# Optimization experiments

Hardware: AMD Instinct MI355X
Metric: run time of the kernel (lower is better)

## Reference

```python
import jax, jax.numpy as jnp
import numpy as np
from jax import lax

C = 64  # filters, reduction=1


def setup_inputs() -> dict:
    key = jax.random.key(0)
    k = jax.random.split(key, 5)
    B, H, W = 16, 64, 64
    x = jax.random.normal(k[0], (B, C, H, W), dtype=jnp.float32)
    # conv_du params (PyTorch Conv2d default init scale ~ U(-s,s), s=1/sqrt(fan_in))
    s = 1.0 / np.sqrt(C * 9)
    w1 = jax.random.uniform(k[1], (C, C, 3, 3), jnp.float32, -s, s)
    b1 = jax.random.uniform(k[2], (C,), jnp.float32, -s, s)
    w2 = jax.random.uniform(k[3], (C, C, 3, 3), jnp.float32, -s, s)
    b2 = jax.random.uniform(k[4], (C,), jnp.float32, -s, s)
    return {"x": x, "w1": w1, "b1": b1, "w2": w2, "b2": b2}


def _normalize_cov(cov, iterN=5):
    # Newton-Schulz iteration for matrix square root, as in SOCA.normalizeCov
    B, ch = cov.shape[0], cov.shape[-1]
    I3 = 3.0 * jnp.eye(ch, dtype=cov.dtype)[None]  # [1,ch,ch], broadcasts over batch
    # normA = 1/3 * sum(cov @ 3I) = sum(cov) per batch
    normA = jnp.sum(cov, axis=(1, 2))  # [B]
    A = cov / normA[:, None, None]
    ZY = 0.5 * (I3 - A)
    Y = jnp.matmul(A, ZY)
    Z = ZY
    for _ in range(1, iterN - 1):  # iterations 1..iterN-2
        ZY = 0.5 * (I3 - jnp.matmul(Z, Y))
        Y = jnp.matmul(Y, ZY)
        Z = jnp.matmul(ZY, Z)
    ZY = 0.5 * jnp.matmul(Y, I3 - jnp.matmul(Z, Y))
    y = ZY * jnp.sqrt(normA)[:, None, None]
    y = jnp.mean(y, axis=1).reshape(B, ch, 1, 1)  # mean over rows -> channel descriptor
    return y


def _conv_same(x, w, b):
    out = lax.conv_general_dilated(
        x, w, window_strides=(1, 1), padding="SAME",
        dimension_numbers=("NCHW", "OIHW", "NCHW"))
    return out + b[None, :, None, None]


def reference(x, w1, b1, w2, b2):
    B, c, h, w = x.shape
    M = h * w
    xf = x.reshape(B, c, M)
    Minv = 1.0 / M
    # I_hat = (1/M) * (I - (1/M) * ones)  -- centering matrix, materialized as in source
    I_hat = Minv * (jnp.eye(M, dtype=x.dtype) - Minv * jnp.ones((M, M), dtype=x.dtype))
    cov = jnp.matmul(jnp.matmul(xf, I_hat), jnp.swapaxes(xf, 1, 2))  # [B,c,c]
    y_cov = _normalize_cov(cov, 5)  # [B,c,1,1]
    y = _conv_same(y_cov, w1, b1)
    y = jax.nn.relu(y)
    y = _conv_same(y, w2, b2)
    y = jax.nn.sigmoid(y)
    return y * x
```

## Files before the change

kernel.cpp:

```cpp
#include <hip/hip_runtime.h>
#include <math.h>

#define KS 16
#define CHUNK 256
#define PART_STRIDE 4160

typedef __attribute__((ext_vector_type(8))) short short8;
typedef __attribute__((ext_vector_type(4))) float floatx4;

__device__ __forceinline__ unsigned short f2bf(float f) {
    unsigned int u = __float_as_uint(f);
    return (unsigned short)((u + 0x7fffu + ((u >> 16) & 1u)) >> 16);
}
__device__ __forceinline__ float bf2f(unsigned short h) {
    return __uint_as_float(((unsigned int)h) << 16);
}
__device__ __forceinline__ int HW(int r, int kb) {
    return ((kb << 6) + (r ^ (kb & 15))) << 3;
}
__device__ __forceinline__ floatx4 mfma_bf16(short8 a, short8 b, floatx4 c) {
    return __builtin_amdgcn_mfma_f32_16x16x32_bf16(a, b, c, 0, 0, 0);
}

__global__ __launch_bounds__(256) void cov_partial_kernel(const float* __restrict__ x,
                                                          float* __restrict__ ws) {
    __shared__ __align__(16) unsigned short xh[64 * CHUNK];
    __shared__ __align__(16) unsigned short xl[64 * CHUNK];
    __shared__ float rs_part[4][64];
    int blk = blockIdx.x, b = blk >> 4, ks = blk & 15;
    int tid = threadIdx.x, lane = tid & 63, wv = tid >> 6;
    const float* xb = x + ((size_t)b * 64) * 4096 + ks * CHUNK;

    int kbw = lane >> 1, wsub = (lane & 1) << 2;
    #pragma unroll
    for (int r = 0; r < 16; ++r) {
        int c = wv * 16 + r;
        float4 v = *reinterpret_cast<const float4*>(xb + (size_t)c * 4096 + lane * 4);
        float vv[4] = {v.x, v.y, v.z, v.w};
        unsigned short hs[4], ls[4];
        #pragma unroll
        for (int q = 0; q < 4; ++q) {
            hs[q] = f2bf(vv[q]);
            ls[q] = f2bf(vv[q] - bf2f(hs[q]));
        }
        int idx = HW(c, kbw) + wsub;
        uint2 u;
        u.x = hs[0] | ((unsigned)hs[1] << 16); u.y = hs[2] | ((unsigned)hs[3] << 16);
        *reinterpret_cast<uint2*>(&xh[idx]) = u;
        u.x = ls[0] | ((unsigned)ls[1] << 16); u.y = ls[2] | ((unsigned)ls[3] << 16);
        *reinterpret_cast<uint2*>(&xl[idx]) = u;
    }
    __syncthreads();

    int g = lane >> 4, rh = lane & 15;
    int ta0 = (wv >> 1) << 1, tc0 = (wv & 1) << 1;
    floatx4 acc[2][2];
    #pragma unroll
    for (int a = 0; a < 2; ++a)
        #pragma unroll
        for (int c = 0; c < 2; ++c)
            acc[a][c] = (floatx4){0.f, 0.f, 0.f, 0.f};

    #pragma unroll
    for (int ks_ = 0; ks_ < 8; ++ks_) {
        int kb = ks_ * 4 + g;
        short8 ah[2], al[2], bh[2], bl[2];
        #pragma unroll
        for (int a = 0; a < 2; ++a) {
            int o = HW(16 * (ta0 + a) + rh, kb);
            ah[a] = *reinterpret_cast<const short8*>(&xh[o]);
            al[a] = *reinterpret_cast<const short8*>(&xl[o]);
        }
        #pragma unroll
        for (int c = 0; c < 2; ++c) {
            int o = HW(16 * (tc0 + c) + rh, kb);
            bh[c] = *reinterpret_cast<const short8*>(&xh[o]);
            bl[c] = *reinterpret_cast<const short8*>(&xl[o]);
        }
        #pragma unroll
        for (int a = 0; a < 2; ++a)
            #pragma unroll
            for (int c = 0; c < 2; ++c) {
                acc[a][c] = mfma_bf16(ah[a], bh[c], acc[a][c]);
                acc[a][c] = mfma_bf16(ah[a], bl[c], acc[a][c]);
                acc[a][c] = mfma_bf16(al[a], bh[c], acc[a][c]);
            }
    }

    float* outp = ws + (size_t)blk * PART_STRIDE;
    #pragma unroll
    for (int a = 0; a < 2; ++a)
        #pragma unroll
        for (int c = 0; c < 2; ++c) {
            int j = 16 * (tc0 + c) + rh;
            int i0 = 16 * (ta0 + a) + 4 * g;
            *reinterpret_cast<float4*>(&outp[j * 64 + i0]) =
                make_float4(acc[a][c][0], acc[a][c][1], acc[a][c][2], acc[a][c][3]);
        }

    {
        float s = 0.f;
        #pragma unroll
        for (int m = 0; m < 8; ++m) {
            int o = HW(lane, wv * 8 + m);
            short8 vh = *reinterpret_cast<const short8*>(&xh[o]);
            short8 vl = *reinterpret_cast<const short8*>(&xl[o]);
            #pragma unroll
            for (int e = 0; e < 8; ++e)
                s += bf2f((unsigned short)vh[e]) + bf2f((unsigned short)vl[e]);
        }
        rs_part[wv][lane] = s;
    }
    __syncthreads();
    if (tid < 64)
        outp[4096 + tid] = rs_part[0][tid] + rs_part[1][tid] + rs_part[2][tid] + rs_part[3][tid];
}

template <int MODE>
__device__ __forceinline__ void mm_pass(const unsigned short (*U)[4096],
                                        const unsigned short (*V)[4096],
                                        unsigned short (*D)[4096], int tid) {
    int lane = tid & 63, wv = tid >> 6;
    int g = lane >> 4, rh = lane & 15;
    int ta = wv & 3, tc0 = (wv >> 2) << 1;
    floatx4 acc[2];
    acc[0] = (floatx4){0.f, 0.f, 0.f, 0.f};
    acc[1] = (floatx4){0.f, 0.f, 0.f, 0.f};

    #pragma unroll
    for (int ks_ = 0; ks_ < 2; ++ks_) {
        int kb = ks_ * 4 + g;
        int ao = HW(16 * ta + rh, kb);
        short8 auh = *reinterpret_cast<const short8*>(&U[0][ao]);
        short8 aul = *reinterpret_cast<const short8*>(&U[1][ao]);
        #pragma unroll
        for (int c = 0; c < 2; ++c) {
            int bo = HW(16 * (tc0 + c) + rh, kb);
            short8 bvh = *reinterpret_cast<const short8*>(&V[0][bo]);
            short8 bvl = *reinterpret_cast<const short8*>(&V[1][bo]);
            acc[c] = mfma_bf16(auh, bvh, acc[c]);
            acc[c] = mfma_bf16(auh, bvl, acc[c]);
            acc[c] = mfma_bf16(aul, bvh, acc[c]);
        }
    }

    int kbi = 2 * ta + (g >> 1);
    int sub = (g & 1) << 2;
    #pragma unroll
    for (int c = 0; c < 2; ++c) {
        int j = 16 * (tc0 + c) + rh;
        unsigned short hs[4], ls[4];
        #pragma unroll
        for (int q = 0; q < 4; ++q) {
            int i = 16 * ta + 4 * g + q;
            float v = acc[c][q];
            if (MODE == 0) v = 0.5f * ((i == j ? 3.0f : 0.0f) - v);
            hs[q] = f2bf(v);
            ls[q] = f2bf(v - bf2f(hs[q]));
        }
        int idx = HW(j, kbi) + sub;
        uint2 u;
        u.x = hs[0] | ((unsigned)hs[1] << 16); u.y = hs[2] | ((unsigned)hs[3] << 16);
        *reinterpret_cast<uint2*>(&D[0][idx]) = u;
        u.x = ls[0] | ((unsigned)ls[1] << 16); u.y = ls[2] | ((unsigned)ls[3] << 16);
        *reinterpret_cast<uint2*>(&D[1][idx]) = u;
    }
    __syncthreads();
}

__global__ __launch_bounds__(512) void ns_kernel(const float* __restrict__ wsin,
                                                 const float* __restrict__ w1,
                                                 const float* __restrict__ b1,
                                                 const float* __restrict__ w2,
                                                 const float* __restrict__ b2,
                                                 float* __restrict__ s_out) {
    __shared__ __align__(16) float buf[4096];
    __shared__ __align__(16) unsigned short planes[5][2][4096];
    __shared__ float w1t[64 * 65];
    __shared__ float w2t[64 * 65];
    __shared__ float red[512];
    __shared__ float part[8][64];
    __shared__ float rsum[64], uvec[64], tvec[64], wvec[64], ych[64], hid[64];
    int b = blockIdx.x, tid = threadIdx.x;

    {
        int o = tid & 63, g8 = tid >> 6;
        #pragma unroll
        for (int q = 0; q < 8; ++q) {
            int i = g8 * 8 + q;
            w1t[i * 65 + o] = w1[(o * 64 + i) * 9 + 4];
            w2t[i * 65 + o] = w2[(o * 64 + i) * 9 + 4];
        }
    }

    const float* base = wsin + (size_t)b * KS * PART_STRIDE;
    #pragma unroll
    for (int r = 0; r < 2; ++r) {
        int e = (r * 512 + tid) * 4;
        floatx4 s4 = (floatx4){0.f, 0.f, 0.f, 0.f};
        for (int k = 0; k < KS; ++k)
            s4 += *reinterpret_cast<const floatx4*>(base + k * PART_STRIDE + e);
        *reinterpret_cast<floatx4*>(&buf[e]) = s4;
    }
    if (tid < 64) {
        float s = 0.f;
        for (int k = 0; k < KS; ++k) s += base[k * PART_STRIDE + 4096 + tid];
        rsum[tid] = s;
    }
    __syncthreads();

    const float invM = 1.0f / 4096.0f;
    float lsum = 0.f;
    #pragma unroll
    for (int r = 0; r < 2; ++r) {
        int e = (r * 512 + tid) * 4;
        int i = e >> 6, j = e & 63;
        floatx4 cv = *reinterpret_cast<const floatx4*>(&buf[e]);
        float mui = rsum[i] * invM;
        #pragma unroll
        for (int q = 0; q < 4; ++q) cv[q] = cv[q] * invM - mui * (rsum[j + q] * invM);
        *reinterpret_cast<floatx4*>(&buf[e]) = cv;
        lsum += cv[0] + cv[1] + cv[2] + cv[3];
    }
    red[tid] = lsum;
    __syncthreads();
    for (int s = 256; s > 0; s >>= 1) {
        if (tid < s) red[tid] += red[tid + s];
        __syncthreads();
    }
    const float normA = red[0];
    const float invNA = 1.0f / normA;

    {
        int r = tid >> 3, oct = tid & 7;
        short8 ah, al, zh, zl;
        #pragma unroll
        for (int q = 0; q < 8; ++q) {
            int j = oct * 8 + q;
            float a = buf[r * 64 + j] * invNA;
            float zy = 0.5f * ((r == j ? 3.0f : 0.0f) - a);
            unsigned short h = f2bf(a);
            ah[q] = (short)h; al[q] = (short)f2bf(a - bf2f(h));
            h = f2bf(zy);
            zh[q] = (short)h; zl[q] = (short)f2bf(zy - bf2f(h));
        }
        int idx = HW(r, oct);
        *reinterpret_cast<short8*>(&planes[0][0][idx]) = ah;
        *reinterpret_cast<short8*>(&planes[0][1][idx]) = al;
        *reinterpret_cast<short8*>(&planes[1][0][idx]) = zh;
        *reinterpret_cast<short8*>(&planes[1][1][idx]) = zl;
    }
    __syncthreads();

    mm_pass<1>(planes[0], planes[1], planes[2], tid);
    int yi = 2, zi = 1, f1 = 3, f2 = 4;
    for (int it = 0; it < 3; ++it) {
        mm_pass<0>(planes[zi], planes[yi], planes[0], tid);
        mm_pass<1>(planes[yi], planes[0], planes[f1], tid);
        mm_pass<1>(planes[0], planes[zi], planes[f2], tid);
        int ny = f1, nz = f2;
        f1 = yi; f2 = zi; yi = ny; zi = nz;
    }

    const unsigned short (*Y)[4096] = planes[yi];
    const unsigned short (*Z)[4096] = planes[zi];
    int ii = tid & 63, grp = tid >> 6;
    {
        int o = HW(ii, grp);
        short8 vh = *reinterpret_cast<const short8*>(&Y[0][o]);
        short8 vl = *reinterpret_cast<const short8*>(&Y[1][o]);
        float s = 0.f;
        #pragma unroll
        for (int e = 0; e < 8; ++e)
            s += bf2f((unsigned short)vh[e]) + bf2f((unsigned short)vl[e]);
        part[grp][ii] = s;
    }
    __syncthreads();
    if (tid < 64) {
        float s = 0.f;
        #pragma unroll
        for (int q = 0; q < 8; ++q) s += part[q][tid];
        uvec[tid] = s;
    }
    __syncthreads();
    {
        int o = HW(ii, grp);
        short8 vh = *reinterpret_cast<const short8*>(&Z[0][o]);
        short8 vl = *reinterpret_cast<const short8*>(&Z[1][o]);
        float s = 0.f;
        #pragma unroll
        for (int e = 0; e < 8; ++e)
            s += (bf2f((unsigned short)vh[e]) + bf2f((unsigned short)vl[e])) * uvec[grp * 8 + e];
        part[grp][ii] = s;
    }
    __syncthreads();
    if (tid < 64) {
        float s = 0.f;
        #pragma unroll
        for (int q = 0; q < 8; ++q) s += part[q][tid];
        tvec[tid] = s;
    }
    __syncthreads();
    {
        int o = HW(ii, grp);
        short8 vh = *reinterpret_cast<const short8*>(&Y[0][o]);
        short8 vl = *reinterpret_cast<const short8*>(&Y[1][o]);
        float s = 0.f;
        #pragma unroll
        for (int e = 0; e < 8; ++e)
            s += (bf2f((unsigned short)vh[e]) + bf2f((unsigned short)vl[e])) * tvec[grp * 8 + e];
        part[grp][ii] = s;
    }
    __syncthreads();
    if (tid < 64) {
        float s = 0.f;
        #pragma unroll
        for (int q = 0; q < 8; ++q) s += part[q][tid];
        wvec[tid] = s;
        ych[tid] = (3.0f * uvec[tid] - s) * (0.5f / 64.0f) * sqrtf(normA);
    }
    __syncthreads();
    if (tid < 64) {
        float t1 = b1[tid];
        for (int i = 0; i < 64; ++i) t1 += w1t[i * 65 + tid] * ych[i];
        hid[tid] = fmaxf(t1, 0.f);
    }
    __syncthreads();
    if (tid < 64) {
        float t2 = b2[tid];
        for (int i = 0; i < 64; ++i) t2 += w2t[i * 65 + tid] * hid[i];
        s_out[b * 64 + tid] = 1.0f / (1.0f + expf(-t2));
    }
}

__global__ __launch_bounds__(256) void scale_kernel(const float* __restrict__ x,
                                                    const float* __restrict__ s,
                                                    float* __restrict__ out, int n4) {
    int idx = blockIdx.x * 256 + threadIdx.x;
    int stride = gridDim.x * 256;
    for (int f = idx; f < n4; f += stride) {
        float sv = s[f >> 10];
        float4 v = reinterpret_cast<const float4*>(x)[f];
        reinterpret_cast<float4*>(out)[f] = make_float4(v.x * sv, v.y * sv, v.z * sv, v.w * sv);
    }
}

extern "C" void kernel_launch(void* const* d_in, const int* in_sizes, int n_in,
                              void* d_out, int out_size, void* d_ws, size_t ws_size,
                              hipStream_t stream) {
    const float* x  = (const float*)d_in[0];
    const float* w1 = (const float*)d_in[1];
    const float* b1 = (const float*)d_in[2];
    const float* w2 = (const float*)d_in[3];
    const float* b2 = (const float*)d_in[4];
    float* out = (float*)d_out;
    float* ws  = (float*)d_ws;
    float* s_area = ws + (size_t)256 * PART_STRIDE;

    cov_partial_kernel<<<dim3(256), dim3(256), 0, stream>>>(x, ws);
    ns_kernel<<<dim3(16), dim3(512), 0, stream>>>(ws, w1, b1, w2, b2, s_area);
    scale_kernel<<<dim3(2048), dim3(256), 0, stream>>>(x, s_area, out, 1048576);
}
```

Measured before the change: 35.79 us.

## Split covariance reduction into separate kernel and fuse independent Newton-Schulz matmuls

Moves the cross-split partial reduction, centering, normalization and bf16 hi/lo conversion out of the 16-block serial NS kernel into a new 64-block kernel. normA is computed analytically from the sum of squared column sums and the row sums instead of a block-wide reduction. The NS kernel grows to 1024 threads and runs the independent Y*ZY and ZY*Z products of each iteration in one pass, with the final vector chain reassociated. The cost is an extra kernel launch and a global round trip for the planes, plus some change in rounding behaviour.

```diff
diff --git a/kernel.cpp b/kernel.cpp
--- a/kernel.cpp
+++ b/kernel.cpp
@@ -1,16 +1,17 @@
 #include <hip/hip_runtime.h>
+#include <hip/hip_bf16.h>
 #include <math.h>
 
 #define KS 16
 #define CHUNK 256
-#define PART_STRIDE 4160
+#define PART_STRIDE 4224
 
 typedef __attribute__((ext_vector_type(8))) short short8;
 typedef __attribute__((ext_vector_type(4))) float floatx4;
 
 __device__ __forceinline__ unsigned short f2bf(float f) {
-    unsigned int u = __float_as_uint(f);
-    return (unsigned short)((u + 0x7fffu + ((u >> 16) & 1u)) >> 16);
+    __hip_bfloat16 h = __float2bfloat16(f);
+    return *reinterpret_cast<unsigned short*>(&h);
 }
 __device__ __forceinline__ float bf2f(unsigned short h) {
     return __uint_as_float(((unsigned int)h) << 16);
@@ -27,15 +28,19 @@
     __shared__ __align__(16) unsigned short xh[64 * CHUNK];
     __shared__ __align__(16) unsigned short xl[64 * CHUNK];
     __shared__ float rs_part[4][64];
+    __shared__ float csp[4][256];
+    __shared__ float red[256];
     int blk = blockIdx.x, b = blk >> 4, ks = blk & 15;
     int tid = threadIdx.x, lane = tid & 63, wv = tid >> 6;
     const float* xb = x + ((size_t)b * 64) * 4096 + ks * CHUNK;
 
     int kbw = lane >> 1, wsub = (lane & 1) << 2;
+    float cs0 = 0.f, cs1 = 0.f, cs2 = 0.f, cs3 = 0.f;
     #pragma unroll
     for (int r = 0; r < 16; ++r) {
         int c = wv * 16 + r;
         float4 v = *reinterpret_cast<const float4*>(xb + (size_t)c * 4096 + lane * 4);
+        cs0 += v.x; cs1 += v.y; cs2 += v.z; cs3 += v.w;
         float vv[4] = {v.x, v.y, v.z, v.w};
         unsigned short hs[4], ls[4];
         #pragma unroll
@@ -50,7 +55,10 @@
         u.x = ls[0] | ((unsigned)ls[1] << 16); u.y = ls[2] | ((unsigned)ls[3] << 16);
         *reinterpret_cast<uint2*>(&xl[idx]) = u;
     }
-    __syncthreads();
+    *reinterpret_cast<float4*>(&csp[wv][lane * 4]) = make_float4(cs0, cs1, cs2, cs3);
+    __syncthreads();
+
+    float cm = csp[0][tid] + csp[1][tid] + csp[2][tid] + csp[3][tid];
 
     int g = lane >> 4, rh = lane & 15;
     int ta0 = (wv >> 1) << 1, tc0 = (wv & 1) << 1;
@@ -111,52 +119,159 @@
         }
         rs_part[wv][lane] = s;
     }
-    __syncthreads();
+    red[tid] = cm * cm;
+    __syncthreads();
+    for (int st = 128; st > 0; st >>= 1) {
+        if (tid < st) red[tid] += red[tid + st];
+        __syncthreads();
+    }
     if (tid < 64)
         outp[4096 + tid] = rs_part[0][tid] + rs_part[1][tid] + rs_part[2][tid] + rs_part[3][tid];
+    if (tid == 0) outp[4160] = red[0];
+}
+
+__global__ __launch_bounds__(256) void reduce_convert_kernel(const float* __restrict__ ws,
+                                                             unsigned short* __restrict__ planesG,
+                                                             float* __restrict__ normAG) {
+    __shared__ float rsum[64];
+    __shared__ float Tsh, normA_sh;
+    int blk = blockIdx.x, b = blk >> 2, q = blk & 3;
+    int tid = threadIdx.x;
+    const float* base = ws + (size_t)b * KS * PART_STRIDE;
+    const float invM = 1.0f / 4096.0f;
+
+    if (tid < 64) {
+        float s = 0.f;
+        for (int k = 0; k < KS; ++k) s += base[k * PART_STRIDE + 4096 + tid];
+        rsum[tid] = s;
+    } else if (tid == 64) {
+        float t = 0.f;
+        for (int k = 0; k < KS; ++k) t += base[k * PART_STRIDE + 4160];
+        Tsh = t;
+    }
+    __syncthreads();
+    if (tid == 0) {
+        float sr = 0.f;
+        for (int i = 0; i < 64; ++i) sr += rsum[i];
+        float nA = (Tsh - sr * sr * invM) * invM;
+        normA_sh = nA;
+        if (q == 0) normAG[b] = nA;
+    }
+    __syncthreads();
+    const float invNA = 1.0f / normA_sh;
+
+    int E = q * 1024 + tid * 4;
+    int i = E >> 6, j0 = E & 63;
+    floatx4 s4 = (floatx4){0.f, 0.f, 0.f, 0.f};
+    for (int k = 0; k < KS; ++k)
+        s4 += *reinterpret_cast<const floatx4*>(base + k * PART_STRIDE + E);
+    float mui = rsum[i] * invM;
+    unsigned short ah[4], al_[4], zh[4], zl[4];
+    #pragma unroll
+    for (int e = 0; e < 4; ++e) {
+        float cv = s4[e] * invM - mui * (rsum[j0 + e] * invM);
+        float a = cv * invNA;
+        float z = 0.5f * (((i == j0 + e) ? 3.0f : 0.0f) - a);
+        unsigned short h = f2bf(a);
+        ah[e] = h; al_[e] = f2bf(a - bf2f(h));
+        h = f2bf(z);
+        zh[e] = h; zl[e] = f2bf(z - bf2f(h));
+    }
+    int kb = j0 >> 3, sub = j0 & 7;
+    int idx = HW(i, kb) + sub;
+    unsigned short* pb = planesG + (size_t)b * 4 * 4096;
+    uint2 u;
+    u.x = ah[0] | ((unsigned)ah[1] << 16); u.y = ah[2] | ((unsigned)ah[3] << 16);
+    *reinterpret_cast<uint2*>(&pb[0 * 4096 + idx]) = u;
+    u.x = al_[0] | ((unsigned)al_[1] << 16); u.y = al_[2] | ((unsigned)al_[3] << 16);
+    *reinterpret_cast<uint2*>(&pb[1 * 4096 + idx]) = u;
+    u.x = zh[0] | ((unsigned)zh[1] << 16); u.y = zh[2] | ((unsigned)zh[3] << 16);
+    *reinterpret_cast<uint2*>(&pb[2 * 4096 + idx]) = u;
+    u.x = zl[0] | ((unsigned)zl[1] << 16); u.y = zl[2] | ((unsigned)zl[3] << 16);
+    *reinterpret_cast<uint2*>(&pb[3 * 4096 + idx]) = u;
 }
 
 template <int MODE>
-__device__ __forceinline__ void mm_pass(const unsigned short (*U)[4096],
-                                        const unsigned short (*V)[4096],
-                                        unsigned short (*D)[4096], int tid) {
+__device__ __forceinline__ void pass_single(const unsigned short (*U)[4096],
+                                            const unsigned short (*V)[4096],
+                                            unsigned short (*D)[4096], int tid) {
     int lane = tid & 63, wv = tid >> 6;
     int g = lane >> 4, rh = lane & 15;
-    int ta = wv & 3, tc0 = (wv >> 2) << 1;
-    floatx4 acc[2];
-    acc[0] = (floatx4){0.f, 0.f, 0.f, 0.f};
-    acc[1] = (floatx4){0.f, 0.f, 0.f, 0.f};
-
+    int ta = wv & 3, tc = wv >> 2;
+    floatx4 acc = (floatx4){0.f, 0.f, 0.f, 0.f};
     #pragma unroll
     for (int ks_ = 0; ks_ < 2; ++ks_) {
         int kb = ks_ * 4 + g;
         int ao = HW(16 * ta + rh, kb);
+        int bo = HW(16 * tc + rh, kb);
         short8 auh = *reinterpret_cast<const short8*>(&U[0][ao]);
         short8 aul = *reinterpret_cast<const short8*>(&U[1][ao]);
-        #pragma unroll
-        for (int c = 0; c < 2; ++c) {
-            int bo = HW(16 * (tc0 + c) + rh, kb);
-            short8 bvh = *reinterpret_cast<const short8*>(&V[0][bo]);
-            short8 bvl = *reinterpret_cast<const short8*>(&V[1][bo]);
-            acc[c] = mfma_bf16(auh, bvh, acc[c]);
-            acc[c] = mfma_bf16(auh, bvl, acc[c]);
-            acc[c] = mfma_bf16(aul, bvh, acc[c]);
-        }
-    }
-
-    int kbi = 2 * ta + (g >> 1);
-    int sub = (g & 1) << 2;
-    #pragma unroll
-    for (int c = 0; c < 2; ++c) {
-        int j = 16 * (tc0 + c) + rh;
+        short8 bvh = *reinterpret_cast<const short8*>(&V[0][bo]);
+        short8 bvl = *reinterpret_cast<const short8*>(&V[1][bo]);
+        acc = mfma_bf16(auh, bvh, acc);
+        acc = mfma_bf16(auh, bvl, acc);
+        acc = mfma_bf16(aul, bvh, acc);
+    }
+    int j = 16 * tc + rh;
+    int kbi = 2 * ta + (g >> 1), sub = (g & 1) << 2;
+    unsigned short hs[4], ls[4];
+    #pragma unroll
+    for (int qq = 0; qq < 4; ++qq) {
+        int i = 16 * ta + 4 * g + qq;
+        float v = acc[qq];
+        if (MODE == 0) v = 0.5f * ((i == j ? 3.0f : 0.0f) - v);
+        hs[qq] = f2bf(v);
+        ls[qq] = f2bf(v - bf2f(hs[qq]));
+    }
+    int idx = HW(j, kbi) + sub;
+    uint2 u;
+    u.x = hs[0] | ((unsigned)hs[1] << 16); u.y = hs[2] | ((unsigned)hs[3] << 16);
+    *reinterpret_cast<uint2*>(&D[0][idx]) = u;
+    u.x = ls[0] | ((unsigned)ls[1] << 16); u.y = ls[2] | ((unsigned)ls[3] << 16);
+    *reinterpret_cast<uint2*>(&D[1][idx]) = u;
+    __syncthreads();
+}
+
+__device__ __forceinline__ void pass_fused(const unsigned short (*Y)[4096],
+                                           const unsigned short (*W)[4096],
+                                           const unsigned short (*Z)[4096],
+                                           unsigned short (*DY)[4096],
+                                           unsigned short (*DZ)[4096], int tid) {
+    int lane = tid & 63, wv = tid >> 6;
+    int g = lane >> 4, rh = lane & 15;
+    const unsigned short (*U)[4096] = (wv < 8) ? Y : W;
+    const unsigned short (*V)[4096] = (wv < 8) ? W : Z;
+    unsigned short (*D)[4096] = (wv < 8) ? DY : DZ;
+    int w8 = wv & 7;
+    int ta0 = (w8 >> 2) << 1, tc = w8 & 3;
+    floatx4 acc[2] = {(floatx4){0.f,0.f,0.f,0.f}, (floatx4){0.f,0.f,0.f,0.f}};
+    #pragma unroll
+    for (int ks_ = 0; ks_ < 2; ++ks_) {
+        int kb = ks_ * 4 + g;
+        int bo = HW(16 * tc + rh, kb);
+        short8 bvh = *reinterpret_cast<const short8*>(&V[0][bo]);
+        short8 bvl = *reinterpret_cast<const short8*>(&V[1][bo]);
+        #pragma unroll
+        for (int a = 0; a < 2; ++a) {
+            int ao = HW(16 * (ta0 + a) + rh, kb);
+            short8 auh = *reinterpret_cast<const short8*>(&U[0][ao]);
+            short8 aul = *reinterpret_cast<const short8*>(&U[1][ao]);
+            acc[a] = mfma_bf16(auh, bvh, acc[a]);
+            acc[a] = mfma_bf16(auh, bvl, acc[a]);
+            acc[a] = mfma_bf16(aul, bvh, acc[a]);
+        }
+    }
+    int j = 16 * tc + rh;
+    #pragma unroll
+    for (int a = 0; a < 2; ++a) {
+        int ta = ta0 + a;
+        int kbi = 2 * ta + (g >> 1), sub = (g & 1) << 2;
         unsigned short hs[4], ls[4];
         #pragma unroll
-        for (int q = 0; q < 4; ++q) {
-            int i = 16 * ta + 4 * g + q;
-            float v = acc[c][q];
-            if (MODE == 0) v = 0.5f * ((i == j ? 3.0f : 0.0f) - v);
-            hs[q] = f2bf(v);
-            ls[q] = f2bf(v - bf2f(hs[q]));
+        for (int qq = 0; qq < 4; ++qq) {
+            float v = acc[a][qq];
+            hs[qq] = f2bf(v);
+            ls[qq] = f2bf(v - bf2f(hs[qq]));
         }
         int idx = HW(j, kbi) + sub;
         uint2 u;
@@ -168,157 +283,101 @@
     __syncthreads();
 }
 
-__global__ __launch_bounds__(512) void ns_kernel(const float* __restrict__ wsin,
-                                                 const float* __restrict__ w1,
-                                                 const float* __restrict__ b1,
-                                                 const float* __restrict__ w2,
-                                                 const float* __restrict__ b2,
-                                                 float* __restrict__ s_out) {
-    __shared__ __align__(16) float buf[4096];
+__device__ __forceinline__ void colsum_stage(const unsigned short (*M)[4096],
+                                             float* dst, float (*part)[64], int tid) {
+    int ii = tid & 63, grp = (tid >> 6) & 7;
+    if (tid < 512) {
+        int o = HW(ii, grp);
+        short8 vh = *reinterpret_cast<const short8*>(&M[0][o]);
+        short8 vl = *reinterpret_cast<const short8*>(&M[1][o]);
+        float s = 0.f;
+        #pragma unroll
+        for (int e = 0; e < 8; ++e)
+            s += bf2f((unsigned short)vh[e]) + bf2f((unsigned short)vl[e]);
+        part[grp][ii] = s;
+    }
+    __syncthreads();
+    if (tid < 64) {
+        float s = 0.f;
+        #pragma unroll
+        for (int q = 0; q < 8; ++q) s += part[q][tid];
+        dst[tid] = s;
+    }
+    __syncthreads();
+}
+
+__device__ __forceinline__ void matvec_stage(const unsigned short (*M)[4096],
+                                             const float* __restrict__ src,
+                                             float* dst, float (*part)[64], int tid) {
+    int ii = tid & 63, grp = (tid >> 6) & 7;
+    if (tid < 512) {
+        int o = HW(ii, grp);
+        short8 vh = *reinterpret_cast<const short8*>(&M[0][o]);
+        short8 vl = *reinterpret_cast<const short8*>(&M[1][o]);
+        float s = 0.f;
+        #pragma unroll
+        for (int e = 0; e < 8; ++e)
+            s += (bf2f((unsigned short)vh[e]) + bf2f((unsigned short)vl[e])) * src[grp * 8 + e];
+        part[grp][ii] = s;
+    }
+    __syncthreads();
+    if (tid < 64) {
+        float s = 0.f;
+        #pragma unroll
+        for (int q = 0; q < 8; ++q) s += part[q][tid];
+        dst[tid] = s;
+    }
+    __syncthreads();
+}
+
+__global__ __launch_bounds__(1024) void ns_kernel(const unsigned short* __restrict__ planesG,
+                                                  const float* __restrict__ normAG,
+                                                  const float* __restrict__ w1,
+                                                  const float* __restrict__ b1,
+                                                  const float* __restrict__ w2,
+                                                  const float* __restrict__ b2,
+                                                  float* __restrict__ s_out) {
     __shared__ __align__(16) unsigned short planes[5][2][4096];
     __shared__ float w1t[64 * 65];
     __shared__ float w2t[64 * 65];
-    __shared__ float red[512];
     __shared__ float part[8][64];
-    __shared__ float rsum[64], uvec[64], tvec[64], wvec[64], ych[64], hid[64];
+    __shared__ float uvec[64], avec[64], pvec[64], wvec[64], ych[64], hid[64];
+    __shared__ float normA_sh;
     int b = blockIdx.x, tid = threadIdx.x;
 
+    {
+        const uint4* src = reinterpret_cast<const uint4*>(planesG + (size_t)b * 4 * 4096);
+        uint4* dst = reinterpret_cast<uint4*>(&planes[0][0][0]);
+        dst[tid] = src[tid];
+        dst[tid + 1024] = src[tid + 1024];
+    }
     {
         int o = tid & 63, g8 = tid >> 6;
         #pragma unroll
-        for (int q = 0; q < 8; ++q) {
-            int i = g8 * 8 + q;
+        for (int q = 0; q < 4; ++q) {
+            int i = g8 * 4 + q;
             w1t[i * 65 + o] = w1[(o * 64 + i) * 9 + 4];
             w2t[i * 65 + o] = w2[(o * 64 + i) * 9 + 4];
         }
     }
-
-    const float* base = wsin + (size_t)b * KS * PART_STRIDE;
-    #pragma unroll
-    for (int r = 0; r < 2; ++r) {
-        int e = (r * 512 + tid) * 4;
-        floatx4 s4 = (floatx4){0.f, 0.f, 0.f, 0.f};
-        for (int k = 0; k < KS; ++k)
-            s4 += *reinterpret_cast<const floatx4*>(base + k * PART_STRIDE + e);
-        *reinterpret_cast<floatx4*>(&buf[e]) = s4;
-    }
-    if (tid < 64) {
-        float s = 0.f;
-        for (int k = 0; k < KS; ++k) s += base[k * PART_STRIDE + 4096 + tid];
-        rsum[tid] = s;
-    }
-    __syncthreads();
-
-    const float invM = 1.0f / 4096.0f;
-    float lsum = 0.f;
-    #pragma unroll
-    for (int r = 0; r < 2; ++r) {
-        int e = (r * 512 + tid) * 4;
-        int i = e >> 6, j = e & 63;
-        floatx4 cv = *reinterpret_cast<const floatx4*>(&buf[e]);
-        float mui = rsum[i] * invM;
-        #pragma unroll
-        for (int q = 0; q < 4; ++q) cv[q] = cv[q] * invM - mui * (rsum[j + q] * invM);
-        *reinterpret_cast<floatx4*>(&buf[e]) = cv;
-        lsum += cv[0] + cv[1] + cv[2] + cv[3];
-    }
-    red[tid] = lsum;
-    __syncthreads();
-    for (int s = 256; s > 0; s >>= 1) {
-        if (tid < s) red[tid] += red[tid + s];
-        __syncthreads();
-    }
-    const float normA = red[0];
-    const float invNA = 1.0f / normA;
-
-    {
-        int r = tid >> 3, oct = tid & 7;
-        short8 ah, al, zh, zl;
-        #pragma unroll
-        for (int q = 0; q < 8; ++q) {
-            int j = oct * 8 + q;
-            float a = buf[r * 64 + j] * invNA;
-            float zy = 0.5f * ((r == j ? 3.0f : 0.0f) - a);
-            unsigned short h = f2bf(a);
-            ah[q] = (short)h; al[q] = (short)f2bf(a - bf2f(h));
-            h = f2bf(zy);
-            zh[q] = (short)h; zl[q] = (short)f2bf(zy - bf2f(h));
-        }
-        int idx = HW(r, oct);
-        *reinterpret_cast<short8*>(&planes[0][0][idx]) = ah;
-        *reinterpret_cast<short8*>(&planes[0][1][idx]) = al;
-        *reinterpret_cast<short8*>(&planes[1][0][idx]) = zh;
-        *reinterpret_cast<short8*>(&planes[1][1][idx]) = zl;
-    }
-    __syncthreads();
-
-    mm_pass<1>(planes[0], planes[1], planes[2], tid);
-    int yi = 2, zi = 1, f1 = 3, f2 = 4;
-    for (int it = 0; it < 3; ++it) {
-        mm_pass<0>(planes[zi], planes[yi], planes[0], tid);
-        mm_pass<1>(planes[yi], planes[0], planes[f1], tid);
-        mm_pass<1>(planes[0], planes[zi], planes[f2], tid);
-        int ny = f1, nz = f2;
-        f1 = yi; f2 = zi; yi = ny; zi = nz;
-    }
-
-    const unsigned short (*Y)[4096] = planes[yi];
-    const unsigned short (*Z)[4096] = planes[zi];
-    int ii = tid & 63, grp = tid >> 6;
-    {
-        int o = HW(ii, grp);
-        short8 vh = *reinterpret_cast<const short8*>(&Y[0][o]);
-        short8 vl = *reinterpret_cast<const short8*>(&Y[1][o]);
-        float s = 0.f;
-        #pragma unroll
-        for (int e = 0; e < 8; ++e)
-            s += bf2f((unsigned short)vh[e]) + bf2f((unsigned short)vl[e]);
-        part[grp][ii] = s;
-    }
-    __syncthreads();
-    if (tid < 64) {
-        float s = 0.f;
-        #pragma unroll
-        for (int q = 0; q < 8; ++q) s += part[q][tid];
-        uvec[tid] = s;
-    }
-    __syncthreads();
-    {
-        int o = HW(ii, grp);
-        short8 vh = *reinterpret_cast<const short8*>(&Z[0][o]);
-        short8 vl = *reinterpret_cast<const short8*>(&Z[1][o]);
-        float s = 0.f;
-        #pragma unroll
-        for (int e = 0; e < 8; ++e)
-            s += (bf2f((unsigned short)vh[e]) + bf2f((unsigned short)vl[e])) * uvec[grp * 8 + e];
-        part[grp][ii] = s;
-    }
-    __syncthreads();
-    if (tid < 64) {
-        float s = 0.f;
-        #pragma unroll
-        for (int q = 0; q < 8; ++q) s += part[q][tid];
-        tvec[tid] = s;
-    }
-    __syncthreads();
-    {
-        int o = HW(ii, grp);
-        short8 vh = *reinterpret_cast<const short8*>(&Y[0][o]);
-        short8 vl = *reinterpret_cast<const short8*>(&Y[1][o]);
-        float s = 0.f;
-        #pragma unroll
-        for (int e = 0; e < 8; ++e)
-            s += (bf2f((unsigned short)vh[e]) + bf2f((unsigned short)vl[e])) * tvec[grp * 8 + e];
-        part[grp][ii] = s;
-    }
-    __syncthreads();
-    if (tid < 64) {
-        float s = 0.f;
-        #pragma unroll
-        for (int q = 0; q < 8; ++q) s += part[q][tid];
-        wvec[tid] = s;
-        ych[tid] = (3.0f * uvec[tid] - s) * (0.5f / 64.0f) * sqrtf(normA);
-    }
+    if (tid == 0) normA_sh = normAG[b];
+    __syncthreads();
+
+    pass_single<1>(planes[0], planes[1], planes[2], tid);
+    pass_single<0>(planes[1], planes[2], planes[0], tid);
+    pass_fused(planes[2], planes[0], planes[1], planes[3], planes[4], tid);
+    pass_single<0>(planes[4], planes[3], planes[1], tid);
+    pass_fused(planes[3], planes[1], planes[4], planes[2], planes[0], tid);
+    pass_single<0>(planes[0], planes[2], planes[3], tid);
+    pass_single<1>(planes[2], planes[3], planes[4], tid);
+
+    colsum_stage(planes[4], uvec, part, tid);
+    matvec_stage(planes[0], uvec, avec, part, tid);
+    matvec_stage(planes[3], avec, pvec, part, tid);
+    matvec_stage(planes[4], pvec, wvec, part, tid);
+
+    if (tid < 64)
+        ych[tid] = (3.0f * uvec[tid] - wvec[tid]) * (0.5f / 64.0f) * sqrtf(normA_sh);
     __syncthreads();
     if (tid < 64) {
         float t1 = b1[tid];
@@ -355,9 +414,12 @@
     const float* b2 = (const float*)d_in[4];
     float* out = (float*)d_out;
     float* ws  = (float*)d_ws;
-    float* s_area = ws + (size_t)256 * PART_STRIDE;
+    unsigned short* planesG = (unsigned short*)(ws + (size_t)256 * PART_STRIDE);
+    float* normAG = (float*)(planesG + (size_t)16 * 4 * 4096);
+    float* s_area = normAG + 16;
 
     cov_partial_kernel<<<dim3(256), dim3(256), 0, stream>>>(x, ws);
-    ns_kernel<<<dim3(16), dim3(512), 0, stream>>>(ws, w1, b1, w2, b2, s_area);
+    reduce_convert_kernel<<<dim3(64), dim3(256), 0, stream>>>(ws, planesG, normAG);
+    ns_kernel<<<dim3(16), dim3(1024), 0, stream>>>(planesG, normAG, w1, b1, w2, b2, s_area);
     scale_kernel<<<dim3(2048), dim3(256), 0, stream>>>(x, s_area, out, 1048576);
 }
```

New measurement: 35.98 us. Within noise of the previous version (+0.5%).

## Run Newton-Schulz with a single wavefront per batch and compute normA analytically

Applied to the files above, without the earlier changes.

Replaces the 512-thread Newton-Schulz kernel with a 64-thread single-wavefront kernel. Each wave computes full 64x64 matmuls with 16 accumulator tiles, so the cross-wave barrier and reduction overhead goes away. The covariance trace normA is derived from a new sum of squared column sums produced in the cov kernel, which removes the block-wide reduction. Conv weights are read directly from global memory instead of being staged in shared memory. The trade-off is much lower parallelism per batch (one wave doing all MFMAs serially) and higher register pressure.

```diff
diff --git a/kernel.cpp b/kernel.cpp
--- a/kernel.cpp
+++ b/kernel.cpp
@@ -1,16 +1,17 @@
 #include <hip/hip_runtime.h>
+#include <hip/hip_bf16.h>
 #include <math.h>
 
 #define KS 16
 #define CHUNK 256
-#define PART_STRIDE 4160
+#define PART_STRIDE 4224
 
 typedef __attribute__((ext_vector_type(8))) short short8;
 typedef __attribute__((ext_vector_type(4))) float floatx4;
 
 __device__ __forceinline__ unsigned short f2bf(float f) {
-    unsigned int u = __float_as_uint(f);
-    return (unsigned short)((u + 0x7fffu + ((u >> 16) & 1u)) >> 16);
+    __hip_bfloat16 h = __float2bfloat16(f);
+    return *reinterpret_cast<unsigned short*>(&h);
 }
 __device__ __forceinline__ float bf2f(unsigned short h) {
     return __uint_as_float(((unsigned int)h) << 16);
@@ -27,15 +28,19 @@
     __shared__ __align__(16) unsigned short xh[64 * CHUNK];
     __shared__ __align__(16) unsigned short xl[64 * CHUNK];
     __shared__ float rs_part[4][64];
+    __shared__ float csp[4][256];
+    __shared__ float red[256];
     int blk = blockIdx.x, b = blk >> 4, ks = blk & 15;
     int tid = threadIdx.x, lane = tid & 63, wv = tid >> 6;
     const float* xb = x + ((size_t)b * 64) * 4096 + ks * CHUNK;
 
     int kbw = lane >> 1, wsub = (lane & 1) << 2;
+    float cs0 = 0.f, cs1 = 0.f, cs2 = 0.f, cs3 = 0.f;
     #pragma unroll
     for (int r = 0; r < 16; ++r) {
         int c = wv * 16 + r;
         float4 v = *reinterpret_cast<const float4*>(xb + (size_t)c * 4096 + lane * 4);
+        cs0 += v.x; cs1 += v.y; cs2 += v.z; cs3 += v.w;
         float vv[4] = {v.x, v.y, v.z, v.w};
         unsigned short hs[4], ls[4];
         #pragma unroll
@@ -50,7 +55,10 @@
         u.x = ls[0] | ((unsigned)ls[1] << 16); u.y = ls[2] | ((unsigned)ls[3] << 16);
         *reinterpret_cast<uint2*>(&xl[idx]) = u;
     }
-    __syncthreads();
+    *reinterpret_cast<float4*>(&csp[wv][lane * 4]) = make_float4(cs0, cs1, cs2, cs3);
+    __syncthreads();
+
+    float cm = csp[0][tid] + csp[1][tid] + csp[2][tid] + csp[3][tid];
 
     int g = lane >> 4, rh = lane & 15;
     int ta0 = (wv >> 1) << 1, tc0 = (wv & 1) << 1;
@@ -111,226 +119,193 @@
         }
         rs_part[wv][lane] = s;
     }
-    __syncthreads();
+    red[tid] = cm * cm;
+    __syncthreads();
+    for (int st = 128; st > 0; st >>= 1) {
+        if (tid < st) red[tid] += red[tid + st];
+        __syncthreads();
+    }
     if (tid < 64)
         outp[4096 + tid] = rs_part[0][tid] + rs_part[1][tid] + rs_part[2][tid] + rs_part[3][tid];
+    if (tid == 0) outp[4160] = red[0];
 }
 
 template <int MODE>
-__device__ __forceinline__ void mm_pass(const unsigned short (*U)[4096],
-                                        const unsigned short (*V)[4096],
-                                        unsigned short (*D)[4096], int tid) {
-    int lane = tid & 63, wv = tid >> 6;
+__device__ __forceinline__ void mm64w(const unsigned short (*U)[4096],
+                                      const unsigned short (*V)[4096],
+                                      unsigned short (*D)[4096], int lane) {
     int g = lane >> 4, rh = lane & 15;
-    int ta = wv & 3, tc0 = (wv >> 2) << 1;
-    floatx4 acc[2];
-    acc[0] = (floatx4){0.f, 0.f, 0.f, 0.f};
-    acc[1] = (floatx4){0.f, 0.f, 0.f, 0.f};
+    floatx4 acc[4][4];
+    #pragma unroll
+    for (int a = 0; a < 4; ++a)
+        #pragma unroll
+        for (int c = 0; c < 4; ++c)
+            acc[a][c] = (floatx4){0.f, 0.f, 0.f, 0.f};
 
     #pragma unroll
     for (int ks_ = 0; ks_ < 2; ++ks_) {
         int kb = ks_ * 4 + g;
-        int ao = HW(16 * ta + rh, kb);
-        short8 auh = *reinterpret_cast<const short8*>(&U[0][ao]);
-        short8 aul = *reinterpret_cast<const short8*>(&U[1][ao]);
-        #pragma unroll
-        for (int c = 0; c < 2; ++c) {
-            int bo = HW(16 * (tc0 + c) + rh, kb);
-            short8 bvh = *reinterpret_cast<const short8*>(&V[0][bo]);
-            short8 bvl = *reinterpret_cast<const short8*>(&V[1][bo]);
-            acc[c] = mfma_bf16(auh, bvh, acc[c]);
-            acc[c] = mfma_bf16(auh, bvl, acc[c]);
-            acc[c] = mfma_bf16(aul, bvh, acc[c]);
-        }
-    }
-
-    int kbi = 2 * ta + (g >> 1);
-    int sub = (g & 1) << 2;
-    #pragma unroll
-    for (int c = 0; c < 2; ++c) {
-        int j = 16 * (tc0 + c) + rh;
-        unsigned short hs[4], ls[4];
+        short8 uh[4], ul[4], vh[4], vl[4];
+        #pragma unroll
+        for (int a = 0; a < 4; ++a) {
+            int o = HW(16 * a + rh, kb);
+            uh[a] = *reinterpret_cast<const short8*>(&U[0][o]);
+            ul[a] = *reinterpret_cast<const short8*>(&U[1][o]);
+        }
+        #pragma unroll
+        for (int c = 0; c < 4; ++c) {
+            int o = HW(16 * c + rh, kb);
+            vh[c] = *reinterpret_cast<const short8*>(&V[0][o]);
+            vl[c] = *reinterpret_cast<const short8*>(&V[1][o]);
+        }
+        #pragma unroll
+        for (int a = 0; a < 4; ++a)
+            #pragma unroll
+            for (int c = 0; c < 4; ++c) {
+                acc[a][c] = mfma_bf16(uh[a], vh[c], acc[a][c]);
+                acc[a][c] = mfma_bf16(uh[a], vl[c], acc[a][c]);
+                acc[a][c] = mfma_bf16(ul[a], vh[c], acc[a][c]);
+            }
+    }
+
+    #pragma unroll
+    for (int a = 0; a < 4; ++a) {
+        int kbi = 2 * a + (g >> 1), sub = (g & 1) << 2;
+        #pragma unroll
+        for (int c = 0; c < 4; ++c) {
+            int j = 16 * c + rh;
+            unsigned short hs[4], ls[4];
+            #pragma unroll
+            for (int qq = 0; qq < 4; ++qq) {
+                int i = 16 * a + 4 * g + qq;
+                float v = acc[a][c][qq];
+                if (MODE == 0) v = 0.5f * ((i == j ? 3.0f : 0.0f) - v);
+                hs[qq] = f2bf(v);
+                ls[qq] = f2bf(v - bf2f(hs[qq]));
+            }
+            int idx = HW(j, kbi) + sub;
+            uint2 u;
+            u.x = hs[0] | ((unsigned)hs[1] << 16); u.y = hs[2] | ((unsigned)hs[3] << 16);
+            *reinterpret_cast<uint2*>(&D[0][idx]) = u;
+            u.x = ls[0] | ((unsigned)ls[1] << 16); u.y = ls[2] | ((unsigned)ls[3] << 16);
+            *reinterpret_cast<uint2*>(&D[1][idx]) = u;
+        }
+    }
+    __syncthreads();
+}
+
+__device__ __forceinline__ float mv64(const unsigned short (*M)[4096],
+                                      const float* __restrict__ src, int lane) {
+    float s = 0.f;
+    #pragma unroll
+    for (int kb = 0; kb < 8; ++kb) {
+        int o = HW(lane, kb);
+        short8 vh = *reinterpret_cast<const short8*>(&M[0][o]);
+        short8 vl = *reinterpret_cast<const short8*>(&M[1][o]);
+        #pragma unroll
+        for (int e = 0; e < 8; ++e)
+            s += (bf2f((unsigned short)vh[e]) + bf2f((unsigned short)vl[e])) * src[kb * 8 + e];
+    }
+    return s;
+}
+
+__global__ __launch_bounds__(64, 1) void ns64_kernel(const float* __restrict__ wsin,
+                                                     const float* __restrict__ w1,
+                                                     const float* __restrict__ b1,
+                                                     const float* __restrict__ w2,
+                                                     const float* __restrict__ b2,
+                                                     float* __restrict__ s_out) {
+    __shared__ __align__(16) unsigned short planes[5][2][4096];
+    __shared__ float rsum[64], uvec[64], avec[64], pvec[64], ych[64], hid[64];
+    int b = blockIdx.x, lane = threadIdx.x;
+    const float invM = 1.0f / 4096.0f;
+    const float* base = wsin + (size_t)b * KS * PART_STRIDE;
+
+    float rs = 0.f;
+    for (int k = 0; k < KS; ++k) rs += base[k * PART_STRIDE + 4096 + lane];
+    rsum[lane] = rs;
+    float sr = rs;
+    #pragma unroll
+    for (int off = 32; off >= 1; off >>= 1) sr += __shfl_xor(sr, off, 64);
+    float T = 0.f;
+    for (int k = 0; k < KS; ++k) T += base[k * PART_STRIDE + 4160];
+    const float normA = (T - sr * sr * invM) * invM;
+    const float invNA = 1.0f / normA;
+    __syncthreads();
+
+    const floatx4* b4 = reinterpret_cast<const floatx4*>(base);
+    #pragma unroll
+    for (int chunk = 0; chunk < 16; ++chunk) {
+        int t = chunk * 64 + lane;
+        floatx4 s4 = (floatx4){0.f, 0.f, 0.f, 0.f};
+        for (int k = 0; k < KS; ++k) s4 += b4[k * (PART_STRIDE / 4) + t];
+        int i = t >> 4, j0 = (t & 15) * 4;
+        float mui = rsum[i] * invM;
+        unsigned short ah[4], al_[4], zh[4], zl[4];
         #pragma unroll
         for (int q = 0; q < 4; ++q) {
-            int i = 16 * ta + 4 * g + q;
-            float v = acc[c][q];
-            if (MODE == 0) v = 0.5f * ((i == j ? 3.0f : 0.0f) - v);
-            hs[q] = f2bf(v);
-            ls[q] = f2bf(v - bf2f(hs[q]));
-        }
-        int idx = HW(j, kbi) + sub;
+            float cv = s4[q] * invM - mui * (rsum[j0 + q] * invM);
+            float a = cv * invNA;
+            float z = 0.5f * (((i == j0 + q) ? 3.0f : 0.0f) - a);
+            unsigned short h = f2bf(a);
+            ah[q] = h; al_[q] = f2bf(a - bf2f(h));
+            h = f2bf(z);
+            zh[q] = h; zl[q] = f2bf(z - bf2f(h));
+        }
+        int idx = HW(i, j0 >> 3) + (j0 & 7);
         uint2 u;
-        u.x = hs[0] | ((unsigned)hs[1] << 16); u.y = hs[2] | ((unsigned)hs[3] << 16);
-        *reinterpret_cast<uint2*>(&D[0][idx]) = u;
-        u.x = ls[0] | ((unsigned)ls[1] << 16); u.y = ls[2] | ((unsigned)ls[3] << 16);
-        *reinterpret_cast<uint2*>(&D[1][idx]) = u;
-    }
-    __syncthreads();
-}
-
-__global__ __launch_bounds__(512) void ns_kernel(const float* __restrict__ wsin,
-                                                 const float* __restrict__ w1,
-                                                 const float* __restrict__ b1,
-                                                 const float* __restrict__ w2,
-                                                 const float* __restrict__ b2,
-                                                 float* __restrict__ s_out) {
-    __shared__ __align__(16) float buf[4096];
-    __shared__ __align__(16) unsigned short planes[5][2][4096];
-    __shared__ float w1t[64 * 65];
-    __shared__ float w2t[64 * 65];
-    __shared__ float red[512];
-    __shared__ float part[8][64];
-    __shared__ float rsum[64], uvec[64], tvec[64], wvec[64], ych[64], hid[64];
-    int b = blockIdx.x, tid = threadIdx.x;
+        u.x = ah[0] | ((unsigned)ah[1] << 16); u.y = ah[2] | ((unsigned)ah[3] << 16);
+        *reinterpret_cast<uint2*>(&planes[0][0][idx]) = u;
+        u.x = al_[0] | ((unsigned)al_[1] << 16); u.y = al_[2] | ((unsigned)al_[3] << 16);
+        *reinterpret_cast<uint2*>(&planes[0][1][idx]) = u;
+        u.x = zh[0] | ((unsigned)zh[1] << 16); u.y = zh[2] | ((unsigned)zh[3] << 16);
+        *reinterpret_cast<uint2*>(&planes[1][0][idx]) = u;
+        u.x = zl[0] | ((unsigned)zl[1] << 16); u.y = zl[2] | ((unsigned)zl[3] << 16);
+        *reinterpret_cast<uint2*>(&planes[1][1][idx]) = u;
+    }
+    __syncthreads();
+
+    mm64w<1>(planes[0], planes[1], planes[2], lane);
+    mm64w<0>(planes[1], planes[2], planes[0], lane);
+    mm64w<1>(planes[2], planes[0], planes[3], lane);
+    mm64w<1>(planes[0], planes[1], planes[4], lane);
+    mm64w<0>(planes[4], planes[3], planes[1], lane);
+    mm64w<1>(planes[3], planes[1], planes[2], lane);
+    mm64w<1>(planes[1], planes[4], planes[0], lane);
+    mm64w<0>(planes[0], planes[2], planes[3], lane);
+    mm64w<1>(planes[2], planes[3], planes[4], lane);
 
     {
-        int o = tid & 63, g8 = tid >> 6;
-        #pragma unroll
-        for (int q = 0; q < 8; ++q) {
-            int i = g8 * 8 + q;
-            w1t[i * 65 + o] = w1[(o * 64 + i) * 9 + 4];
-            w2t[i * 65 + o] = w2[(o * 64 + i) * 9 + 4];
-        }
-    }
-
-    const float* base = wsin + (size_t)b * KS * PART_STRIDE;
-    #pragma unroll
-    for (int r = 0; r < 2; ++r) {
-        int e = (r * 512 + tid) * 4;
-        floatx4 s4 = (floatx4){0.f, 0.f, 0.f, 0.f};
-        for (int k = 0; k < KS; ++k)
-            s4 += *reinterpret_cast<const floatx4*>(base + k * PART_STRIDE + e);
-        *reinterpret_cast<floatx4*>(&buf[e]) = s4;
-    }
-    if (tid < 64) {
         float s = 0.f;
-        for (int k = 0; k < KS; ++k) s += base[k * PART_STRIDE + 4096 + tid];
-        rsum[tid] = s;
-    }
-    __syncthreads();
-
-    const float invM = 1.0f / 4096.0f;
-    float lsum = 0.f;
-    #pragma unroll
-    for (int r = 0; r < 2; ++r) {
-        int e = (r * 512 + tid) * 4;
-        int i = e >> 6, j = e & 63;
-        floatx4 cv = *reinterpret_cast<const floatx4*>(&buf[e]);
-        float mui = rsum[i] * invM;
-        #pragma unroll
-        for (int q = 0; q < 4; ++q) cv[q] = cv[q] * invM - mui * (rsum[j + q] * invM);
-        *reinterpret_cast<floatx4*>(&buf[e]) = cv;
-        lsum += cv[0] + cv[1] + cv[2] + cv[3];
-    }
-    red[tid] = lsum;
-    __syncthreads();
-    for (int s = 256; s > 0; s >>= 1) {
-        if (tid < s) red[tid] += red[tid + s];
-        __syncthreads();
-    }
-    const float normA = red[0];
-    const float invNA = 1.0f / normA;
-
-    {
-        int r = tid >> 3, oct = tid & 7;
-        short8 ah, al, zh, zl;
-        #pragma unroll
-        for (int q = 0; q < 8; ++q) {
-            int j = oct * 8 + q;
-            float a = buf[r * 64 + j] * invNA;
-            float zy = 0.5f * ((r == j ? 3.0f : 0.0f) - a);
-            unsigned short h = f2bf(a);
-            ah[q] = (short)h; al[q] = (short)f2bf(a - bf2f(h));
-            h = f2bf(zy);
-            zh[q] = (short)h; zl[q] = (short)f2bf(zy - bf2f(h));
-        }
-        int idx = HW(r, oct);
-        *reinterpret_cast<short8*>(&planes[0][0][idx]) = ah;
-        *reinterpret_cast<short8*>(&planes[0][1][idx]) = al;
-        *reinterpret_cast<short8*>(&planes[1][0][idx]) = zh;
-        *reinterpret_cast<short8*>(&planes[1][1][idx]) = zl;
-    }
-    __syncthreads();
-
-    mm_pass<1>(planes[0], planes[1], planes[2], tid);
-    int yi = 2, zi = 1, f1 = 3, f2 = 4;
-    for (int it = 0; it < 3; ++it) {
-        mm_pass<0>(planes[zi], planes[yi], planes[0], tid);
-        mm_pass<1>(planes[yi], planes[0], planes[f1], tid);
-        mm_pass<1>(planes[0], planes[zi], planes[f2], tid);
-        int ny = f1, nz = f2;
-        f1 = yi; f2 = zi; yi = ny; zi = nz;
-    }
-
-    const unsigned short (*Y)[4096] = planes[yi];
-    const unsigned short (*Z)[4096] = planes[zi];
-    int ii = tid & 63, grp = tid >> 6;
-    {
-        int o = HW(ii, grp);
-        short8 vh = *reinterpret_cast<const short8*>(&Y[0][o]);
-        short8 vl = *reinterpret_cast<const short8*>(&Y[1][o]);
-        float s = 0.f;
-        #pragma unroll
-        for (int e = 0; e < 8; ++e)
-            s += bf2f((unsigned short)vh[e]) + bf2f((unsigned short)vl[e]);
-        part[grp][ii] = s;
-    }
-    __syncthreads();
-    if (tid < 64) {
-        float s = 0.f;
-        #pragma unroll
-        for (int q = 0; q < 8; ++q) s += part[q][tid];
-        uvec[tid] = s;
-    }
-    __syncthreads();
-    {
-        int o = HW(ii, grp);
-        short8 vh = *reinterpret_cast<const short8*>(&Z[0][o]);
-        short8 vl = *reinterpret_cast<const short8*>(&Z[1][o]);
-        float s = 0.f;
-        #pragma unroll
-        for (int e = 0; e < 8; ++e)
-            s += (bf2f((unsigned short)vh[e]) + bf2f((unsigned short)vl[e])) * uvec[grp * 8 + e];
-        part[grp][ii] = s;
-    }
-    __syncthreads();
-    if (tid < 64) {
-        float s = 0.f;
-        #pragma unroll
-        for (int q = 0; q < 8; ++q) s += part[q][tid];
-        tvec[tid] = s;
-    }
-    __syncthreads();
-    {
-        int o = HW(ii, grp);
-        short8 vh = *reinterpret_cast<const short8*>(&Y[0][o]);
-        short8 vl = *reinterpret_cast<const short8*>(&Y[1][o]);
-        float s = 0.f;
-        #pragma unroll
-        for (int e = 0; e < 8; ++e)
-            s += (bf2f((unsigned short)vh[e]) + bf2f((unsigned short)vl[e])) * tvec[grp * 8 + e];
-        part[grp][ii] = s;
-    }
-    __syncthreads();
-    if (tid < 64) {
-        float s = 0.f;
-        #pragma unroll
-        for (int q = 0; q < 8; ++q) s += part[q][tid];
-        wvec[tid] = s;
-        ych[tid] = (3.0f * uvec[tid] - s) * (0.5f / 64.0f) * sqrtf(normA);
-    }
-    __syncthreads();
-    if (tid < 64) {
-        float t1 = b1[tid];
-        for (int i = 0; i < 64; ++i) t1 += w1t[i * 65 + tid] * ych[i];
-        hid[tid] = fmaxf(t1, 0.f);
-    }
-    __syncthreads();
-    if (tid < 64) {
-        float t2 = b2[tid];
-        for (int i = 0; i < 64; ++i) t2 += w2t[i * 65 + tid] * hid[i];
-        s_out[b * 64 + tid] = 1.0f / (1.0f + expf(-t2));
-    }
+        #pragma unroll
+        for (int kb = 0; kb < 8; ++kb) {
+            int o = HW(lane, kb);
+            short8 vh = *reinterpret_cast<const short8*>(&planes[4][0][o]);
+            short8 vl = *reinterpret_cast<const short8*>(&planes[4][1][o]);
+            #pragma unroll
+            for (int e = 0; e < 8; ++e)
+                s += bf2f((unsigned short)vh[e]) + bf2f((unsigned short)vl[e]);
+        }
+        uvec[lane] = s;
+    }
+    __syncthreads();
+    avec[lane] = mv64(planes[0], uvec, lane);
+    __syncthreads();
+    pvec[lane] = mv64(planes[3], avec, lane);
+    __syncthreads();
+    float wv_ = mv64(planes[4], pvec, lane);
+    ych[lane] = (3.0f * uvec[lane] - wv_) * (0.5f / 64.0f) * sqrtf(normA);
+    __syncthreads();
+
+    float t1 = b1[lane];
+    for (int i2 = 0; i2 < 64; ++i2)
+        t1 += w1[(lane * 64 + i2) * 9 + 4] * ych[i2];
+    hid[lane] = fmaxf(t1, 0.f);
+    __syncthreads();
+    float t2 = b2[lane];
+    for (int i2 = 0; i2 < 64; ++i2)
+        t2 += w2[(lane * 64 + i2) * 9 + 4] * hid[i2];
+    s_out[b * 64 + lane] = 1.0f / (1.0f + expf(-t2));
 }
 
 __global__ __launch_bounds__(256) void scale_kernel(const float* __restrict__ x,
@@ -358,6 +333,6 @@
     float* s_area = ws + (size_t)256 * PART_STRIDE;
 
     cov_partial_kernel<<<dim3(256), dim3(256), 0, stream>>>(x, ws);
-    ns_kernel<<<dim3(16), dim3(512), 0, stream>>>(ws, w1, b1, w2, b2, s_area);
+    ns64_kernel<<<dim3(16), dim3(64), 0, stream>>>(ws, w1, b1, w2, b2, s_area);
     scale_kernel<<<dim3(2048), dim3(256), 0, stream>>>(x, s_area, out, 1048576);
 }
```

New measurement: 50.43 us. +40.9%, slower.
